# Kernel optimization log

Measured on AMD Instinct MI355X. Metric: run time of the kernel, lower is better.

## Reference

```python
import jax, jax.numpy as jnp
import numpy as np

L, B, D, H = 128, 4, 768, 300
NT, NR = 7, 12  # ner tags, relation types
EPS = 1e-5


def _cummax(v):
    # torch: cumsum(softmax(v, -1), -1)
    return jnp.cumsum(jax.nn.softmax(v, axis=-1), axis=-1)


def _layernorm(v, g, b):
    mu = jnp.mean(v, axis=-1, keepdims=True)
    var = jnp.var(v, axis=-1, keepdims=True)
    return (v - mu) * jax.lax.rsqrt(var + EPS) * g + b


def setup_inputs() -> dict:
    key = jax.random.key(0)
    ks = jax.random.split(key, 24)
    s = lambda fan_in: 1.0 / np.sqrt(fan_in)
    u = lambda k, shape, sc: jax.random.uniform(k, shape, jnp.float32, -sc, sc)
    inp = {
        "x": jax.random.normal(ks[0], (L, B, D), jnp.float32),
        "mask": jnp.ones((L, B), jnp.float32),
        # PFN_Unit
        "W_ih": u(ks[1], (5 * H, D), s(D)), "b_ih": u(ks[2], (5 * H,), s(D)),
        "W_hh": u(ks[3], (5 * H, H), s(H)), "b_hh": u(ks[4], (5 * H,), s(H)),
        "W_tr": u(ks[5], (H, 3 * H), s(3 * H)), "b_tr": u(ks[6], (H,), s(3 * H)),
        # NERUnit
        "n_W": u(ks[7], (H, 2 * H), s(2 * H)), "n_b": u(ks[8], (H,), s(2 * H)),
        "ner_hW": u(ks[9], (H, 3 * H), s(3 * H)), "ner_hb": u(ks[10], (H,), s(3 * H)),
        "ner_g": jnp.ones((H,), jnp.float32), "ner_beta": jnp.zeros((H,), jnp.float32),
        "ner_tW": u(ks[11], (NT, H), s(H)), "ner_tb": u(ks[12], (NT,), s(H)),
        # ReUnit
        "r_W": u(ks[13], (H, 2 * H), s(2 * H)), "r_b": u(ks[14], (H,), s(2 * H)),
        "re_hW": u(ks[15], (H, 3 * H), s(3 * H)), "re_hb": u(ks[16], (H,), s(3 * H)),
        "re_g": jnp.ones((H,), jnp.float32), "re_beta": jnp.zeros((H,), jnp.float32),
        "re_tW": u(ks[17], (NR, H), s(H)), "re_tb": u(ks[18], (NR,), s(H)),
    }
    return inp


def _encoder(x, W_ih, b_ih, W_hh, b_hh, W_tr, b_tr):
    pre = jnp.einsum('lbd,gd->lbg', x, W_ih) + b_ih  # precompute input transform [L,B,5H]

    def step(carry, gx):
        h, c_in = carry
        gates = gx + h @ W_hh.T + b_hh
        c, eg_cin, rg_cin, eg_c, rg_c = jnp.split(gates, 5, axis=1)
        eg_cin, rg_cin = 1.0 - _cummax(eg_cin), _cummax(rg_cin)
        eg_c, rg_c = 1.0 - _cummax(eg_c), _cummax(rg_c)
        c = jnp.tanh(c)
        ov_c = rg_c * eg_c
        up_c, dn_c = rg_c - ov_c, eg_c - ov_c
        ov_i = rg_cin * eg_cin
        up_i, dn_i = rg_cin - ov_i, eg_cin - ov_i
        share = ov_i * c_in + ov_c * c
        c_re = up_i * c_in + up_c * c + share
        c_ner = dn_i * c_in + dn_c * c + share
        c_out = jnp.concatenate([c_re, c_ner, share], axis=-1) @ W_tr.T + b_tr
        h_out = jnp.tanh(c_out)
        return (h_out, c_out), (jnp.tanh(c_ner), jnp.tanh(c_re), jnp.tanh(share))

    h0 = jnp.zeros((x.shape[1], W_hh.shape[1]), x.dtype)
    _, (h_ner, h_re, h_share) = jax.lax.scan(step, (h0, h0), pre)
    return h_ner, h_re, h_share  # each [L,B,H]


def _pair_unit(h_task, h_share, mask, gW, gb, hW, hb, ln_g, ln_b, tW, tb, diag):
    length = h_task.shape[0]
    # global feature: tanh(Linear(cat(share, task))), max over time
    h_glob = jnp.tanh(jnp.concatenate([h_share, h_task], axis=-1) @ gW.T + gb)  # [L,B,H]
    g = jnp.max(h_glob, axis=0)  # [B,H]
    # pairwise feature [L,L,B,3H] = cat(start, end, global)
    st = jnp.broadcast_to(h_task[:, None], (length, length) + h_task.shape[1:])
    en = jnp.broadcast_to(h_task[None, :], (length, length) + h_task.shape[1:])
    gb4 = jnp.broadcast_to(g, (length, length) + g.shape)
    feat = jnp.concatenate([st, en, gb4], axis=-1)
    out = _layernorm(feat @ hW.T + hb, ln_g, ln_b)
    out = jax.nn.elu(out)  # eval mode: dropout is identity
    out = jax.nn.sigmoid(out @ tW.T + tb)  # [L,L,B,T]
    # mask
    m = mask[:, None, :] * mask[None, :, :]  # [L,L,B]
    if diag:
        m = m * jnp.triu(jnp.ones((length, length), out.dtype))[:, :, None]
    return out * m[..., None]


def reference(x, mask, W_ih, b_ih, W_hh, b_hh, W_tr, b_tr,
              n_W, n_b, ner_hW, ner_hb, ner_g, ner_beta, ner_tW, ner_tb,
              r_W, r_b, re_hW, re_hb, re_g, re_beta, re_tW, re_tb):
    h_ner, h_re, h_share = _encoder(x, W_ih, b_ih, W_hh, b_hh, W_tr, b_tr)
    ner = _pair_unit(h_ner, h_share, mask, n_W, n_b, ner_hW, ner_hb,
                     ner_g, ner_beta, ner_tW, ner_tb, diag=True)
    re = _pair_unit(h_re, h_share, mask, r_W, r_b, re_hW, re_hb,
                    re_g, re_beta, re_tW, re_tb, diag=False)
    return ner, re
```

## Files before the change

kernel.cpp:

```cpp
#include <hip/hip_runtime.h>

#define LLEN 128
#define BB 4
#define DD 768
#define HH 300
#define G5 1500
#define H3 900
#define NTT 7
#define NRR 12
#define NCHB 10
#define RPB 150
#define OPB 30

#define C_WIH  0
#define C_X    1152000
#define C_WHH2 1545216
#define C_WTR2 1995216
#define F_BIH  2265216
#define F_BTR  2266720
#define F_PRE  2267040
#define F_HG0  (F_PRE)
#define F_HG1  (F_PRE+153600)
#define F_A0   (F_PRE+307200)
#define F_E0   (F_PRE+460800)
#define F_GF0  (F_PRE+616832)
#define F_GF1  (F_PRE+618048)
#define F_HNER (F_PRE+768000)
#define F_HRE  (F_HNER+153600)
#define F_HSH  (F_HRE+153600)
#define F_A1   0
#define F_E1   153600
#define F_AUX  (F_HSH+153600)
#define P_CPUB 192000
#define AUXB   2432
#define AUX_FL 9728
#define WS_NEED_BYTES ((size_t)(F_AUX+11776)*4)

typedef unsigned short u16;
typedef unsigned int u32;
typedef float f4 __attribute__((ext_vector_type(4)));
typedef int i4 __attribute__((ext_vector_type(4)));

__device__ __forceinline__ float bf2f(u16 u) {
  union { u32 i; float f; } v; v.i = ((u32)u) << 16; return v.f;
}
__device__ __forceinline__ u16 f2bf(float f) {
  union { float f; u32 i; } v; v.f = f;
  u32 r = v.i + 0x7fffu + ((v.i >> 16) & 1u);
  return (u16)(r >> 16);
}
__device__ __forceinline__ float ldin(const void* p, int i, bool f32) {
  return f32 ? ((const float*)p)[i] : bf2f(((const u16*)p)[i]);
}
__device__ __forceinline__ bool is32(const void* mk) {
  return ((const u16*)mk)[0] == 0;
}
__device__ __forceinline__ float wsum(float x) {
  #pragma unroll
  for (int d = 1; d < 64; d <<= 1) x += __shfl_xor(x, d);
  return x;
}
__device__ __forceinline__ void astore(float* p, float v) {
  union { float f; int i; } u; u.f = v;
  __hip_atomic_store((int*)p, u.i, __ATOMIC_RELAXED, __HIP_MEMORY_SCOPE_AGENT);
}
__device__ __forceinline__ void gbar(int* flag, int tid, int target) {
  __syncthreads();
  if (tid == 0) {
    __builtin_amdgcn_s_waitcnt(0);
    __hip_atomic_fetch_add(flag, 1, __ATOMIC_RELAXED, __HIP_MEMORY_SCOPE_AGENT);
    int it = 0;
    while (__hip_atomic_load(flag, __ATOMIC_RELAXED, __HIP_MEMORY_SCOPE_AGENT) < target) {
      __builtin_amdgcn_s_sleep(1);
      if (++it > 50000) break;
    }
  }
  __syncthreads();
}
__device__ __forceinline__ f4 ld4x(const f4* p, int mode) {
  f4 v;
  if (mode)
    asm volatile("global_load_dwordx4 %0, %1, off sc0\n\ts_waitcnt vmcnt(0)"
                 : "=v"(v) : "v"(p) : "memory");
  else
    asm volatile("global_load_dwordx4 %0, %1, off sc0 sc1\n\ts_waitcnt vmcnt(0)"
                 : "=v"(v) : "v"(p) : "memory");
  return v;
}
__device__ __forceinline__ float ld1x(const float* p, int mode) {
  float v;
  if (mode)
    asm volatile("global_load_dword %0, %1, off sc0\n\ts_waitcnt vmcnt(0)"
                 : "=v"(v) : "v"(p) : "memory");
  else
    asm volatile("global_load_dword %0, %1, off sc0 sc1\n\ts_waitcnt vmcnt(0)"
                 : "=v"(v) : "v"(p) : "memory");
  return v;
}
__device__ __forceinline__ int ldix(const int* p, int mode) {
  int v;
  if (mode)
    asm volatile("global_load_dword %0, %1, off sc0\n\ts_waitcnt vmcnt(0)"
                 : "=v"(v) : "v"(p) : "memory");
  else
    asm volatile("global_load_dword %0, %1, off sc0 sc1\n\ts_waitcnt vmcnt(0)"
                 : "=v"(v) : "v"(p) : "memory");
  return v;
}
__device__ __forceinline__ void exst(float* p, float v, int mode) {
  if (mode) *p = v; else astore(p, v);
}
__device__ __forceinline__ void ld9(const float* base,
                                    f4& a0, f4& a1, f4& a2, f4& a3, f4& a4,
                                    f4& a5, f4& a6, f4& a7, f4& a8) {
  asm volatile(
    "global_load_dwordx4 %0, %9, off sc0\n\t"
    "global_load_dwordx4 %1, %9, off offset:16 sc0\n\t"
    "global_load_dwordx4 %2, %9, off offset:32 sc0\n\t"
    "global_load_dwordx4 %3, %9, off offset:64 sc0\n\t"
    "global_load_dwordx4 %4, %9, off offset:80 sc0\n\t"
    "global_load_dwordx4 %5, %9, off offset:96 sc0\n\t"
    "global_load_dwordx4 %6, %9, off offset:128 sc0\n\t"
    "global_load_dwordx4 %7, %9, off offset:144 sc0\n\t"
    "global_load_dwordx4 %8, %9, off offset:160 sc0\n\t"
    "s_waitcnt vmcnt(0)"
    : "=&v"(a0), "=&v"(a1), "=&v"(a2), "=&v"(a3), "=&v"(a4),
      "=&v"(a5), "=&v"(a6), "=&v"(a7), "=&v"(a8)
    : "v"(base) : "memory");
}
__device__ __forceinline__ int poll10(const int* slots, int tok, int mode) {
  i4 a, b, c;
  if (mode)
    asm volatile("global_load_dwordx4 %0, %3, off sc0\n\t"
                 "global_load_dwordx4 %1, %4, off sc0\n\t"
                 "global_load_dwordx4 %2, %5, off sc0\n\t"
                 "s_waitcnt vmcnt(0)"
                 : "=&v"(a), "=&v"(b), "=&v"(c)
                 : "v"(slots), "v"(slots + 4), "v"(slots + 8) : "memory");
  else
    asm volatile("global_load_dwordx4 %0, %3, off sc0 sc1\n\t"
                 "global_load_dwordx4 %1, %4, off sc0 sc1\n\t"
                 "global_load_dwordx4 %2, %5, off sc0 sc1\n\t"
                 "s_waitcnt vmcnt(0)"
                 : "=&v"(a), "=&v"(b), "=&v"(c)
                 : "v"(slots), "v"(slots + 4), "v"(slots + 8) : "memory");
  return (a.x >= tok) & (a.y >= tok) & (a.z >= tok) & (a.w >= tok) &
         (b.x >= tok) & (b.y >= tok) & (b.z >= tok) & (b.w >= tok) &
         (c.x >= tok) & (c.y >= tok);
}
__device__ __forceinline__ void sbar(int* slots, int ch, int tok, int tid, int mode) {
  asm volatile("s_waitcnt vmcnt(0)" ::: "memory");
  __syncthreads();
  if (tid == 0) {
    if (mode) slots[ch] = tok;
    else __hip_atomic_store(slots + ch, tok, __ATOMIC_RELAXED, __HIP_MEMORY_SCOPE_AGENT);
  }
  if (tid < 64) {
    int it = 0;
    while (!poll10(slots, tok, mode)) {
      __builtin_amdgcn_s_sleep(1);
      if (++it > 5000) break;
    }
  }
  __syncthreads();
}
__device__ __forceinline__ void sbarA(int* slots, int* abf, int ch, int tok, int tid,
                                      volatile int* s_fail) {
  asm volatile("s_waitcnt vmcnt(0)" ::: "memory");
  __syncthreads();
  if (tid == 0)
    __hip_atomic_store(slots + ch, tok, __ATOMIC_RELAXED, __HIP_MEMORY_SCOPE_AGENT);
  if (tid < 64) {
    int it = 0;
    while (!poll10(slots, tok, 0)) {
      __builtin_amdgcn_s_sleep(1);
      ++it;
      if ((it & 255) == 0 &&
          __hip_atomic_load(abf, __ATOMIC_RELAXED, __HIP_MEMORY_SCOPE_AGENT) != 0) {
        *s_fail = 1; break;
      }
      if (it > 8000) {
        __hip_atomic_store(abf, 1, __ATOMIC_RELAXED, __HIP_MEMORY_SCOPE_AGENT);
        *s_fail = 1; break;
      }
    }
  }
  __syncthreads();
}
__device__ __forceinline__ int claim_bc(int* cl, int nb) {
  unsigned xcd;
  asm volatile("s_getreg_b32 %0, hwreg(HW_REG_XCC_ID)" : "=s"(xcd));
  xcd &= 7u;
  int rank = __hip_atomic_fetch_add(cl + xcd, 1, __ATOMIC_RELAXED, __HIP_MEMORY_SCOPE_AGENT);
  __hip_atomic_fetch_add(cl + 8, 1, __ATOMIC_RELAXED, __HIP_MEMORY_SCOPE_AGENT);
  int it = 0;
  while (__hip_atomic_load(cl + 8, __ATOMIC_RELAXED, __HIP_MEMORY_SCOPE_AGENT) < nb) {
    __builtin_amdgcn_s_sleep(2);
    if (++it > 100000) break;
  }
  int base = 0;
  for (unsigned x = 0; x < xcd; ++x)
    base += __hip_atomic_load(cl + x, __ATOMIC_RELAXED, __HIP_MEMORY_SCOPE_AGENT) / NCHB;
  int cnt = __hip_atomic_load(cl + xcd, __ATOMIC_RELAXED, __HIP_MEMORY_SCOPE_AGENT);
  int slot = base + rank / NCHB;
  return (rank < (cnt / NCHB) * NCHB && slot < BB) ? (slot * 16 + rank % NCHB) : -1;
}

__global__ void k_canon(const void* xo, const void* mk, const void* Wih, const void* bih,
                        const void* Whh, const void* bhh, const void* Wtr, const void* btr,
                        float* ws) {
  bool f32 = is32(mk);
  int piece = blockIdx.y;
  int i0 = blockIdx.x * 256 + threadIdx.x;
  int stride = gridDim.x * 256;
  switch (piece) {
    case 0: if (!f32) for (int i = i0; i < 1152000; i += stride) ws[C_WIH + i] = ldin(Wih, i, f32); break;
    case 1: if (!f32) for (int i = i0; i < 393216; i += stride) ws[C_X + i] = ldin(xo, i, f32); break;
    case 2: for (int i = i0; i < 225000; i += stride) {
      int k2 = i / G5, out = i - k2 * G5;
      float2 v;
      v.x = ldin(Whh, out * HH + 2 * k2, f32);
      v.y = ldin(Whh, out * HH + 2 * k2 + 1, f32);
      ((float2*)(ws + C_WHH2))[i] = v;
    } break;
    case 3: for (int i = i0; i < 135000; i += stride) {
      int k2 = i / HH, out = i - k2 * HH;
      float2 v;
      v.x = ldin(Wtr, out * H3 + 2 * k2, f32);
      v.y = ldin(Wtr, out * H3 + 2 * k2 + 1, f32);
      ((float2*)(ws + C_WTR2))[i] = v;
    } break;
    case 4: for (int i = i0; i < 1824; i += stride) {
      if (i < 1504) ws[F_BIH + i] = (i < G5) ? ldin(bih, i, f32) + ldin(bhh, i, f32) : 0.f;
      else { int j = i - 1504; ws[F_BTR + j] = (j < HH) ? ldin(btr, j, f32) : 0.f; }
    } break;
    case 5: for (int i = i0; i < 11776; i += stride) {
      if (i < AUX_FL) ws[F_AUX + i] = 0.f;
      else {
        int* ip = (int*)(ws + F_AUX + AUX_FL);
        __hip_atomic_store(ip + (i - AUX_FL), 0, __ATOMIC_RELAXED, __HIP_MEMORY_SCOPE_AGENT);
      }
    } break;
  }
}

__global__ void k_pre2(const void* xo, const void* Wo, const void* mk,
                       const float* cX, const float* cW, const float* biasf, float* pre) {
  bool f32 = is32(mk);
  const float* X = f32 ? (const float*)xo : cX;
  const float* W = f32 ? (const float*)Wo : cW;
  __shared__ __align__(16) float xl[8 * DD];
  int tid = threadIdx.x;
  int lb0 = (blockIdx.x >> 1) * 8;
  int half = blockIdx.x & 1;
  for (int e = tid; e < 8 * DD; e += 256) xl[e] = X[(size_t)lb0 * DD + e];
  __syncthreads();
  for (int j = half * 750 + tid; j < half * 750 + 750; j += 256) {
    const float4* w = (const float4*)(W + (size_t)j * DD);
    float acc[8] = {0.f, 0.f, 0.f, 0.f, 0.f, 0.f, 0.f, 0.f};
    #pragma unroll 2
    for (int k = 0; k < DD / 4; ++k) {
      float4 u = w[k];
      #pragma unroll
      for (int r = 0; r < 8; ++r) {
        const float4 p = *(const float4*)(xl + r * DD + k * 4);
        acc[r] += u.x * p.x + u.y * p.y + u.z * p.z + u.w * p.w;
      }
    }
    float bias = biasf[j];
    #pragma unroll
    for (int r = 0; r < 8; ++r) pre[(size_t)(lb0 + r) * G5 + j] = acc[r] + bias;
  }
}

__global__ void __launch_bounds__(512, 2) k_scanA(const float* pre, const float2* W2h, const float2* W2t,
                                                  const float* btrf, float* hner, float* hre, float* hsh,
                                                  float* aux, float* xw) {
  __shared__ __align__(16) float ga_l[1504];
  __shared__ __align__(16) float vv_l[1204];
  __shared__ __align__(16) float tnh_l[304];
  __shared__ __align__(16) float cat_l[904];
  __shared__ __align__(16) float ci_l[304];
  __shared__ __align__(16) float ps[512];
  __shared__ __align__(16) float h_loc[32];
  __shared__ int s_bc;
  __shared__ int s_fail;
  int tid = threadIdx.x;
  int* ibase = (int*)(aux + AUX_FL);
  if (tid == 0) { s_bc = claim_bc(ibase, (int)gridDim.x); s_fail = 0; }
  __syncthreads();
  int bc = s_bc;
  if (bc < 0) return;
  int b = bc >> 4, ch = bc & 15;
  int* slots = ibase + 32 + b * 64;
  int* abf   = slots + 24;
  int* done  = ibase + 1536;

  if (ch < 2) {
    float* pb0 = xw + (size_t)ch * 96000 + b * 24000;
    for (int i = tid; i < 3000; i += 512) {
      int row = i >> 1, col = 10 + (i & 1);
      pb0[row * 16 + col] = 0.f;
    }
  }

  int o0 = 3 * tid;
  float2 wh2[45];
  if (tid < 500) {
    #pragma unroll
    for (int j = 0; j < 3; ++j)
      #pragma unroll
      for (int kk = 0; kk < 15; ++kk)
        wh2[j * 15 + kk] = W2h[(size_t)(ch * 15 + kk) * G5 + (o0 + j)];
  }
  int o2 = tid % OPB, jj = tid / OPB;
  float2 wt[29];
  int k2b = jj * 29;
  int k2e = (k2b + 29 < 450) ? (k2b + 29) : 450;
  int nk2 = k2e - k2b;
  if (tid < 480) {
    const float2* wp = W2t + (size_t)k2b * HH + (ch * OPB + o2);
    #pragma unroll
    for (int q = 0; q < 29; ++q) if (q < nk2) wt[q] = wp[(size_t)q * HH];
  }
  float pv0 = 0.f, pv1 = 0.f, pv2 = 0.f;
  if (tid < 500) {
    const float* pr = pre + (size_t)b * G5 + o0;
    pv0 = pr[0]; pv1 = pr[1]; pv2 = pr[2];
  }
  __syncthreads();

  for (int t = 0; t < LLEN; ++t) {
    int buf = t & 1;
    float* pb = xw + (size_t)buf * 96000 + b * 24000;
    if (t > 0) {
      if (tid < 500) {
        float2 h2[15];
        #pragma unroll
        for (int kk = 0; kk < 15; ++kk) h2[kk] = *(const float2*)(h_loc + 2 * kk);
        #pragma unroll
        for (int j = 0; j < 3; ++j) {
          float acc = 0.f;
          #pragma unroll
          for (int kk = 0; kk < 15; ++kk)
            acc += wh2[j * 15 + kk].x * h2[kk].x + wh2[j * 15 + kk].y * h2[kk].y;
          pb[(size_t)(o0 + j) * 16 + ch] = acc;
        }
      }
      sbarA(slots, abf, ch, t, tid, &s_fail);
      if (s_fail) return;
      if (tid < 500) {
        f4 a0, a1, a2, a3, a4, a5, a6, a7, a8;
        ld9(pb + (size_t)o0 * 16, a0, a1, a2, a3, a4, a5, a6, a7, a8);
        ga_l[o0]     = pv0 + (((a0.x + a0.y) + (a0.z + a0.w)) +
                              ((a1.x + a1.y) + (a1.z + a1.w)) +
                              ((a2.x + a2.y) + (a2.z + a2.w)));
        ga_l[o0 + 1] = pv1 + (((a3.x + a3.y) + (a3.z + a3.w)) +
                              ((a4.x + a4.y) + (a4.z + a4.w)) +
                              ((a5.x + a5.y) + (a5.z + a5.w)));
        ga_l[o0 + 2] = pv2 + (((a6.x + a6.y) + (a6.z + a6.w)) +
                              ((a7.x + a7.y) + (a7.z + a7.w)) +
                              ((a8.x + a8.y) + (a8.z + a8.w)));
      }
      if (tid < 75) {
        const float* cp = xw + P_CPUB + (size_t)(((t - 1) & 1) * 4 + b) * 304;
        f4 v = ld4x((const f4*)cp + tid, 1);
        *(f4*)(ci_l + 4 * tid) = v;
      }
    } else {
      if (tid < 500) { ga_l[o0] = pv0; ga_l[o0 + 1] = pv1; ga_l[o0 + 2] = pv2; }
    }
    __syncthreads();
    if (tid < HH) tnh_l[tid] = tanhf(ga_l[tid]);
    {
      int w = tid >> 6, ln = tid & 63;
      if (w >= 4) {
        int c = w - 3;
        const float* g = ga_l + c * 300;
        int e0 = ln * 5;
        float ex0 = 0.f, ex1 = 0.f, ex2 = 0.f, ex3 = 0.f, ex4 = 0.f;
        if (ln < 60) {
          ex0 = __expf(g[e0]); ex1 = __expf(g[e0 + 1]); ex2 = __expf(g[e0 + 2]);
          ex3 = __expf(g[e0 + 3]); ex4 = __expf(g[e0 + 4]);
        }
        float p = ((ex0 + ex1) + (ex2 + ex3)) + ex4;
        float inc = p;
        #pragma unroll
        for (int d = 1; d < 64; d <<= 1) { float o = __shfl_up(inc, d); if (ln >= d) inc += o; }
        float S = __shfl(inc, 59);
        float invS = 1.f / S;
        float run = inc - p;
        if (ln < 60) {
          float* vv = vv_l + (c - 1) * 300 + e0;
          run += ex0; vv[0] = run * invS;
          run += ex1; vv[1] = run * invS;
          run += ex2; vv[2] = run * invS;
          run += ex3; vv[3] = run * invS;
          run += ex4; vv[4] = run * invS;
        }
      }
    }
    if (t + 1 < LLEN && tid < 500) {
      const float* pr = pre + ((size_t)(t + 1) * BB + b) * G5 + o0;
      pv0 = pr[0]; pv1 = pr[1]; pv2 = pr[2];
    }
    __syncthreads();
    if (tid < HH) {
      float c = tnh_l[tid];
      float v0 = vv_l[tid], v1 = vv_l[300 + tid], v2 = vv_l[600 + tid], v3 = vv_l[900 + tid];
      float eg_cin = 1.f - v0, rg_cin = v1, eg_c = 1.f - v2, rg_c = v3;
      float ci = (t > 0) ? ci_l[tid] : 0.f;
      float ov_c = rg_c * eg_c;
      float up_c = rg_c - ov_c, dn_c = eg_c - ov_c;
      float ov_i = rg_cin * eg_cin;
      float up_i = rg_cin - ov_i, dn_i = eg_cin - ov_i;
      float share = ov_i * ci + ov_c * c;
      float c_re  = up_i * ci + up_c * c + share;
      float c_ner = dn_i * ci + dn_c * c + share;
      cat_l[tid] = c_re; cat_l[HH + tid] = c_ner; cat_l[2 * HH + tid] = share;
      int sb = ch * OPB;
      if (tid >= sb && tid < sb + OPB) {
        size_t ob = ((size_t)t * BB + b) * HH + tid;
        hner[ob] = tanhf(c_ner); hre[ob] = tanhf(c_re); hsh[ob] = tanhf(share);
      }
    }
    __syncthreads();
    if (tid < 480) {
      float acc = 0.f;
      #pragma unroll
      for (int q = 0; q < 29; ++q)
        if (q < nk2) acc += wt[q].x * cat_l[2 * (k2b + q)] + wt[q].y * cat_l[2 * (k2b + q) + 1];
      ps[tid] = acc;
    }
    __syncthreads();
    if (tid < OPB) {
      float co = btrf[ch * OPB + tid];
      #pragma unroll
      for (int q = 0; q < 16; ++q) co += ps[q * OPB + tid];
      h_loc[tid] = tanhf(co);
      float* cp = xw + P_CPUB + (size_t)(buf * 4 + b) * 304;
      cp[ch * OPB + tid] = co;
    }
    __syncthreads();
  }
  if (tid == 0 && s_fail == 0)
    __hip_atomic_fetch_add(done + b, 1, __ATOMIC_RELAXED, __HIP_MEMORY_SCOPE_AGENT);
}

__global__ void __launch_bounds__(512, 2) k_scanB(const float* pre, const float2* W2h, const float2* W2t,
                                                  const float* btrf, float* hner, float* hre, float* hsh,
                                                  float* aux) {
  __shared__ __align__(16) float h_l[304];
  __shared__ __align__(16) float ci_l[304];
  __shared__ __align__(16) float ga_l[1504];
  __shared__ __align__(16) float cat_l[904];
  __shared__ __align__(16) float ps[512];
  __shared__ __align__(16) float sums_l[8];
  __shared__ float exv[160];
  __shared__ int s_bc, s_mode, s_skip;
  int tid = threadIdx.x;
  int* ibase = (int*)(aux + AUX_FL);
  int* cl2 = ibase + 640;
  if (tid == 0) s_bc = claim_bc(cl2, (int)gridDim.x);
  __syncthreads();
  int bc = s_bc;
  if (bc < 0) return;
  int b = bc >> 4, ch = bc & 15;
  int* done = ibase + 1536;
  if (tid == 0)
    s_skip = (__hip_atomic_load(done + b, __ATOMIC_RELAXED, __HIP_MEMORY_SCOPE_AGENT) == NCHB);
  __syncthreads();
  if (s_skip) return;
  int s = ch >> 1;
  int r0 = ch * RPB;
  float* gb   = aux + b * AUXB;
  float* cb   = gb + 1504;
  float* hb   = gb + 1808;
  float* sums = gb + 2112;
  int* slotsA = ibase + 672 + b * 64;
  int* slotsB = slotsA + 16;
  int* atf    = slotsA + 32;

  {
    float* tst = gb + 2240;
    int* seflag = (int*)(gb + 2272);
    if (ch == 0 && tid == 0) tst[0] = 1.0f;
    gbar(atf + 0, tid, NCHB);
    if (tid == 0) { float w1 = ld1x(tst, 1); (void)w1; }
    gbar(atf + 1, tid, NCHB);
    if (ch == 0 && tid == 0) { tst[0] = 2.0f; __builtin_amdgcn_s_waitcnt(0); }
    if (ch == 1 && tid == 0)
      __hip_atomic_fetch_add(seflag, 1, __ATOMIC_RELAXED, __HIP_MEMORY_SCOPE_WORKGROUP);
    gbar(atf + 2, tid, NCHB);
    if (tid == 0) {
      float w2 = ld1x(tst, 1);
      int fv = ldix(seflag, 1);
      if (w2 != 2.0f || fv != 1)
        __hip_atomic_fetch_or(atf + 4, 1, __ATOMIC_RELAXED, __HIP_MEMORY_SCOPE_AGENT);
    }
    gbar(atf + 3, tid, NCHB);
    if (tid == 0)
      s_mode = (__hip_atomic_load(atf + 4, __ATOMIC_RELAXED, __HIP_MEMORY_SCOPE_AGENT) == 0) ? 1 : 0;
    __syncthreads();
  }
  int mode = s_mode;

  int j = tid / RPB, r = tid - j * RPB;
  int o2 = tid % OPB, jj = tid / OPB;
  int kb = j * 100;

  float2 wh[50];
  if (tid < 450) {
    const float2* wp = W2h + (size_t)(j * 50) * G5 + (r0 + r);
    #pragma unroll
    for (int kk = 0; kk < 50; ++kk) wh[kk] = wp[(size_t)kk * G5];
  }
  float2 wt[29];
  int k2b = jj * 29;
  int k2e = (k2b + 29 < 450) ? (k2b + 29) : 450;
  int nk2 = k2e - k2b;
  if (tid < 480) {
    const float2* wp = W2t + (size_t)k2b * HH + (ch * OPB + o2);
    #pragma unroll
    for (int q = 0; q < 29; ++q) if (q < nk2) wt[q] = wp[(size_t)q * HH];
  }
  float pv = 0.f;
  if (tid < RPB) pv = pre[(size_t)b * G5 + r0 + tid];
  __syncthreads();

  for (int t = 0; t < LLEN; ++t) {
    if (t > 0) {
      if (tid < 75)       { f4 v = ld4x((const f4*)hb + tid, mode); *(f4*)(h_l + 4 * tid) = v; }
      else if (tid < 150) { int q = tid - 75; f4 v = ld4x((const f4*)cb + q, mode); *(f4*)(ci_l + 4 * q) = v; }
      __syncthreads();
    }
    if (tid < 450) {
      float acc = (j == 0) ? pv : 0.f;
      if (t > 0) {
        #pragma unroll
        for (int kk = 0; kk < 50; ++kk)
          acc += wh[kk].x * h_l[kb + 2 * kk] + wh[kk].y * h_l[kb + 2 * kk + 1];
      }
      ps[tid] = acc;
    }
    __syncthreads();
    if (tid < RPB) {
      float g = ps[tid] + ps[RPB + tid] + ps[2 * RPB + tid];
      if (s == 0) exst(gb + r0 + tid, tanhf(g), mode);
      else exv[tid] = __expf(g);
    }
    if (s > 0) {
      __syncthreads();
      if (tid < 30) {
        int base2 = tid * 5;
        float e0 = exv[base2], e1 = exv[base2 + 1], e2 = exv[base2 + 2],
              e3 = exv[base2 + 3], e4 = exv[base2 + 4];
        float p = ((e0 + e1) + (e2 + e3)) + e4;
        float inc = p;
        #pragma unroll
        for (int d = 1; d < 32; d <<= 1) { float o = __shfl_up(inc, d); if (tid >= d) inc += o; }
        float tot = __shfl(inc, 29);
        float run = inc - p;
        run += e0; exst(gb + r0 + base2,     run, mode);
        run += e1; exst(gb + r0 + base2 + 1, run, mode);
        run += e2; exst(gb + r0 + base2 + 2, run, mode);
        run += e3; exst(gb + r0 + base2 + 3, run, mode);
        run += e4; exst(gb + r0 + base2 + 4, run, mode);
        if (tid == 0) exst(sums + (ch - 2), tot, mode);
      }
    }
    sbar(slotsA, ch, t + 1, tid, mode);
    if (tid < 375)      { f4 v = ld4x((const f4*)gb + tid, mode); *(f4*)(ga_l + 4 * tid) = v; }
    else if (tid < 377) { int q = tid - 375; f4 v = ld4x((const f4*)sums + q, mode); *(f4*)(sums_l + 4 * q) = v; }
    float pvn = 0.f;
    if (t + 1 < LLEN && tid < RPB) pvn = pre[((size_t)(t + 1) * BB + b) * G5 + r0 + tid];
    __syncthreads();
    if (tid < HH) {
      float c = ga_l[tid];
      float v[4];
      #pragma unroll
      for (int s1 = 0; s1 < 4; ++s1) {
        float raw = ga_l[(s1 + 1) * HH + tid];
        float off = (tid >= RPB) ? sums_l[2 * s1] : 0.f;
        float S = sums_l[2 * s1] + sums_l[2 * s1 + 1];
        v[s1] = (raw + off) / S;
      }
      float eg_cin = 1.f - v[0], rg_cin = v[1], eg_c = 1.f - v[2], rg_c = v[3];
      float ci = (t > 0) ? ci_l[tid] : 0.f;
      float ov_c = rg_c * eg_c;
      float up_c = rg_c - ov_c, dn_c = eg_c - ov_c;
      float ov_i = rg_cin * eg_cin;
      float up_i = rg_cin - ov_i, dn_i = eg_cin - ov_i;
      float share = ov_i * ci + ov_c * c;
      float c_re  = up_i * ci + up_c * c + share;
      float c_ner = dn_i * ci + dn_c * c + share;
      cat_l[tid] = c_re; cat_l[HH + tid] = c_ner; cat_l[2 * HH + tid] = share;
      int sb = ch * OPB;
      if (tid >= sb && tid < sb + OPB) {
        size_t ob = ((size_t)t * BB + b) * HH + tid;
        hner[ob] = tanhf(c_ner); hre[ob] = tanhf(c_re); hsh[ob] = tanhf(share);
      }
    }
    __syncthreads();
    if (tid < 480) {
      float acc = 0.f;
      #pragma unroll
      for (int q = 0; q < 29; ++q)
        if (q < nk2) acc += wt[q].x * cat_l[2 * (k2b + q)] + wt[q].y * cat_l[2 * (k2b + q) + 1];
      ps[tid] = acc;
    }
    __syncthreads();
    if (tid < OPB) {
      float co = btrf[ch * OPB + tid];
      #pragma unroll
      for (int q = 0; q < 16; ++q) co += ps[q * OPB + tid];
      exst(cb + ch * OPB + tid, co, mode);
      exst(hb + ch * OPB + tid, tanhf(co), mode);
    }
    if (t + 1 < LLEN) sbar(slotsB, ch, t + 1, tid, mode);
    pv = pvn;
  }
}

__global__ void k_post(const float* hsh, const float* hner, const float* hre,
                       const void* nW, const void* nb, const void* rW, const void* rb,
                       const void* nhW, const void* nhb, const void* rhW, const void* rhb,
                       const void* mk, float* hg0, float* hg1,
                       float* A0, float* E0, float* A1, float* E1) {
  bool f32 = is32(mk);
  int role = blockIdx.x >> 8;
  int sub  = blockIdx.x & 255;
  int task = sub >> 7;
  int lb0 = (sub & 127) * 4;
  __shared__ __align__(16) float buf[2400];
  int tid = threadIdx.x;
  if (role == 0) {
    const float* tsk = task ? hre : hner;
    const void* gWo = task ? rW : nW;
    const void* gbo = task ? rb : nb;
    float* hg = task ? hg1 : hg0;
    for (int e = tid; e < 2400; e += 320) {
      int rr = e / 600, c = e - rr * 600;
      buf[e] = (c < HH) ? hsh[(size_t)(lb0 + rr) * HH + c] : tsk[(size_t)(lb0 + rr) * HH + (c - HH)];
    }
    __syncthreads();
    if (tid < HH) {
      float bias = ldin(gbo, tid, f32);
      float acc[4] = {bias, bias, bias, bias};
      if (f32) {
        const float4* row = (const float4*)((const float*)gWo + (size_t)tid * 600);
        #pragma unroll 2
        for (int k = 0; k < 150; ++k) {
          float4 u = row[k];
          #pragma unroll
          for (int rr = 0; rr < 4; ++rr) {
            const float4 cv = *(const float4*)(buf + rr * 600 + 4 * k);
            acc[rr] += u.x * cv.x + u.y * cv.y + u.z * cv.z + u.w * cv.w;
          }
        }
      } else {
        for (int k = 0; k < 600; ++k) {
          float w = ldin(gWo, tid * 600 + k, f32);
          #pragma unroll
          for (int rr = 0; rr < 4; ++rr) acc[rr] += w * buf[rr * 600 + k];
        }
      }
      #pragma unroll
      for (int rr = 0; rr < 4; ++rr) hg[(size_t)(lb0 + rr) * HH + tid] = tanhf(acc[rr]);
    }
  } else {
    const float* tsk = task ? hre : hner;
    const void* hWo = task ? rhW : nhW;
    const void* hbo = task ? rhb : nhb;
    float* A = task ? A1 : A0;
    float* E = task ? E1 : E0;
    for (int e = tid; e < 1200; e += 320) {
      int rr = e / 300, c = e - rr * 300;
      buf[e] = tsk[(size_t)(lb0 + rr) * HH + c];
    }
    __syncthreads();
    if (tid < HH) {
      float bias = ldin(hbo, tid, f32);
      float a[4] = {bias, bias, bias, bias};
      float ev[4] = {0.f, 0.f, 0.f, 0.f};
      if (f32) {
        const float4* r1 = (const float4*)((const float*)hWo + (size_t)tid * H3);
        const float4* r2 = (const float4*)((const float*)hWo + (size_t)tid * H3 + HH);
        #pragma unroll 2
        for (int k = 0; k < 75; ++k) {
          float4 u = r1[k], w2 = r2[k];
          #pragma unroll
          for (int rr = 0; rr < 4; ++rr) {
            const float4 tv = *(const float4*)(buf + rr * 300 + 4 * k);
            a[rr]  += u.x * tv.x + u.y * tv.y + u.z * tv.z + u.w * tv.w;
            ev[rr] += w2.x * tv.x + w2.y * tv.y + w2.z * tv.z + w2.w * tv.w;
          }
        }
      } else {
        for (int k = 0; k < HH; ++k) {
          float w1 = ldin(hWo, tid * H3 + k, f32);
          float w2 = ldin(hWo, tid * H3 + HH + k, f32);
          #pragma unroll
          for (int rr = 0; rr < 4; ++rr) {
            a[rr] += w1 * buf[rr * 300 + k];
            ev[rr] += w2 * buf[rr * 300 + k];
          }
        }
      }
      #pragma unroll
      for (int rr = 0; rr < 4; ++rr) {
        A[(size_t)(lb0 + rr) * HH + tid] = a[rr];
        E[(size_t)(lb0 + rr) * HH + tid] = ev[rr];
      }
    }
  }
}

__global__ void k_gmf(const float* hg0, const float* hg1, const void* nhW, const void* rhW,
                      const void* mk, float* Gf0, float* Gf1) {
  bool f32 = is32(mk);
  int task = blockIdx.x >> 2, b = blockIdx.x & 3;
  const float* hg = task ? hg1 : hg0;
  const void* hWo = task ? rhW : nhW;
  float* Gf = task ? Gf1 : Gf0;
  __shared__ __align__(16) float gl[304];
  int tid = threadIdx.x;
  if (tid < HH) {
    float m = -1e30f;
    for (int l = 0; l < LLEN; ++l) m = fmaxf(m, hg[((size_t)l * BB + b) * HH + tid]);
    gl[tid] = m;
  }
  __syncthreads();
  if (tid < HH) {
    float acc = 0.f;
    if (f32) {
      const float4* row = (const float4*)((const float*)hWo + (size_t)tid * H3 + 600);
      #pragma unroll 5
      for (int k = 0; k < 75; ++k) {
        float4 u = row[k];
        const float4 gv = *(const float4*)(gl + 4 * k);
        acc += u.x * gv.x + u.y * gv.y + u.z * gv.z + u.w * gv.w;
      }
    } else {
      for (int k = 0; k < HH; ++k) acc += gl[k] * ldin(hWo, tid * H3 + 600 + k, f32);
    }
    Gf[b * HH + tid] = acc;
  }
}

__global__ void __launch_bounds__(256) k_pair7(const float* A0, const float* E0, const float* Gf0,
                                               const void* lg0, const void* lb0_, const void* tW0, const void* tb0,
                                               const float* A1, const float* E1, const float* Gf1,
                                               const void* lg1, const void* lb1_, const void* tW1, const void* tb1,
                                               const void* mk, void* outv) {
  __shared__ float lg_l[304], lb_l[304], tb_l[16];
  __shared__ float tw_l[3616];
  bool f32 = is32(mk);
  int tau = blockIdx.x >> 11;
  int bid = blockIdx.x & 2047;
  int i = bid >> 4;
  int j0 = (bid & 15) << 3;
  int T = tau ? NRR : NTT;
  int diag = tau ? 0 : 1;
  int Toff = tau ? 458752 : 0;
  int tid = threadIdx.x;
  int b = tid >> 6, ln = tid & 63;
  if (diag && j0 + 7 < i) {
    if (ln < T) {
      #pragma unroll
      for (int dj = 0; dj < 8; ++dj) {
        size_t obase = (size_t)Toff + ((size_t)(i * LLEN + j0 + dj) * BB + b) * T;
        if (f32) ((float*)outv)[obase + ln] = 0.f;
        else ((u16*)outv)[obase + ln] = 0;
      }
    }
    return;
  }
  const float* A  = tau ? A1 : A0;
  const float* E  = tau ? E1 : E0;
  const float* Gf = tau ? Gf1 : Gf0;
  const void* lgo = tau ? lg1 : lg0;
  const void* lbo = tau ? lb1_ : lb0_;
  const void* tWo = tau ? tW1 : tW0;
  const void* tbo = tau ? tb1 : tb0;
  for (int i2 = tid; i2 < HH; i2 += 256) { lg_l[i2] = ldin(lgo, i2, f32); lb_l[i2] = ldin(lbo, i2, f32); }
  for (int i2 = tid; i2 < T * HH; i2 += 256) tw_l[i2] = ldin(tWo, i2, f32);
  if (tid < T) tb_l[tid] = ldin(tbo, tid, f32);
  __syncthreads();
  const float* ar = A  + (size_t)(i * BB + b) * HH;
  const float* gr = Gf + (size_t)b * HH;
  bool ok4 = ln < 44;
  float a0 = ar[ln]       + gr[ln];
  float a1 = ar[64 + ln]  + gr[64 + ln];
  float a2 = ar[128 + ln] + gr[128 + ln];
  float a3 = ar[192 + ln] + gr[192 + ln];
  float a4 = ok4 ? (ar[256 + ln] + gr[256 + ln]) : 0.f;
  float mi = ldin(mk, i * BB + b, f32);
  for (int dj = 0; dj < 8; ++dj) {
    int jx = j0 + dj;
    const float* er = E + (size_t)(jx * BB + b) * HH;
    float u0 = a0 + er[ln];
    float u1 = a1 + er[64 + ln];
    float u2 = a2 + er[128 + ln];
    float u3 = a3 + er[192 + ln];
    float u4 = ok4 ? (a4 + er[256 + ln]) : 0.f;
    float s1 = ((u0 + u1) + (u2 + u3)) + u4;
    float s2 = ((u0 * u0 + u1 * u1) + (u2 * u2 + u3 * u3)) + u4 * u4;
    #pragma unroll
    for (int d = 1; d < 64; d <<= 1) { s1 += __shfl_xor(s1, d); s2 += __shfl_xor(s2, d); }
    float mean = s1 * (1.f / 300.f);
    float var = s2 * (1.f / 300.f) - mean * mean;
    float rstd = rsqrtf(var + 1e-5f);
    {
      float y;
      y = (u0 - mean) * rstd * lg_l[ln]       + lb_l[ln];       u0 = (y > 0.f) ? y : __expf(y) - 1.f;
      y = (u1 - mean) * rstd * lg_l[64 + ln]  + lb_l[64 + ln];  u1 = (y > 0.f) ? y : __expf(y) - 1.f;
      y = (u2 - mean) * rstd * lg_l[128 + ln] + lb_l[128 + ln]; u2 = (y > 0.f) ? y : __expf(y) - 1.f;
      y = (u3 - mean) * rstd * lg_l[192 + ln] + lb_l[192 + ln]; u3 = (y > 0.f) ? y : __expf(y) - 1.f;
      if (ok4) {
        y = (u4 - mean) * rstd * lg_l[256 + ln] + lb_l[256 + ln];
        u4 = (y > 0.f) ? y : __expf(y) - 1.f;
      }
    }
    float m = mi * ldin(mk, jx * BB + b, f32);
    if (diag && jx < i) m = 0.f;
    size_t obase = (size_t)Toff + ((size_t)(i * LLEN + jx) * BB + b) * T;
    float mine = 0.f;
    for (int t = 0; t < T; ++t) {
      const float* twr = tw_l + t * HH;
      float s = u0 * twr[ln] + u1 * twr[64 + ln] + u2 * twr[128 + ln] + u3 * twr[192 + ln];
      if (ok4) s += u4 * twr[256 + ln];
      s = wsum(s);
      s += tb_l[t];
      float o = m / (1.f + __expf(-s));
      mine = (ln == t) ? o : mine;
    }
    if (ln < T) {
      if (f32) ((float*)outv)[obase + ln] = mine;
      else ((u16*)outv)[obase + ln] = f2bf(mine);
    }
  }
}

__global__ void k_sent(const void* mk, const void* xo, void* outv, int hostcode) {
  __shared__ int bad;
  if (threadIdx.x == 0) bad = 0;
  __syncthreads();
  bool f32 = is32(mk);
  for (int i = threadIdx.x; i < 4096; i += 256) {
    float v = ldin(xo, i, f32);
    if (!(v == v) || fabsf(v) > 1e6f) bad = 1;
  }
  __syncthreads();
  if (threadIdx.x == 0) {
    float code = (float)hostcode;
    if (bad) code = fmaxf(code, 88.f);
    if (code > 0.f) {
      if (f32) ((float*)outv)[0] = code;
      else ((u16*)outv)[0] = f2bf(code);
    }
  }
}

extern "C" void kernel_launch(void* const* d_in, const int* in_sizes, int n_in,
                              void* d_out, int out_size, void* d_ws, size_t ws_size,
                              hipStream_t stream) {
  const void* x    = d_in[0];
  const void* mask = d_in[1];
  const void* Wih  = d_in[2];
  const void* bih  = d_in[3];
  const void* Whh  = d_in[4];
  const void* bhh  = d_in[5];
  const void* Wtr  = d_in[6];
  const void* btr  = d_in[7];
  const void* nW   = d_in[8];
  const void* nb   = d_in[9];
  const void* nhW  = d_in[10];
  const void* nhb  = d_in[11];
  const void* ng   = d_in[12];
  const void* nbe  = d_in[13];
  const void* ntW  = d_in[14];
  const void* ntb  = d_in[15];
  const void* rW   = d_in[16];
  const void* rb   = d_in[17];
  const void* rhW  = d_in[18];
  const void* rhb  = d_in[19];
  const void* rg   = d_in[20];
  const void* rbe  = d_in[21];
  const void* rtW  = d_in[22];
  const void* rtb  = d_in[23];
  float* ws = (float*)d_ws;

  static const int exp_sz[24] = {393216, 512, 1152000, 1500, 450000, 1500, 270000, 300,
                                 180000, 300, 270000, 300, 300, 300, 2100, 7,
                                 180000, 300, 270000, 300, 300, 300, 3600, 12};
  int hostcode = 0;
  if (n_in != 24) hostcode = 890;
  else {
    for (int ii = 0; ii < 24; ++ii)
      if (in_sizes[ii] != exp_sz[ii]) { hostcode = 900 + ii; break; }
  }
  if (hostcode == 0 && out_size != 1245184) hostcode = 880;
  if (hostcode == 0 && ws_size < WS_NEED_BYTES) hostcode = 1099;

  dim3 gc(512, 6);
  k_canon<<<gc, 256, 0, stream>>>(x, mask, Wih, bih, Whh, bhh, Wtr, btr, ws);
  k_pre2<<<128, 256, 0, stream>>>(x, Wih, mask, ws + C_X, ws + C_WIH, ws + F_BIH, ws + F_PRE);
  k_scanA<<<128, 512, 0, stream>>>(ws + F_PRE, (const float2*)(ws + C_WHH2), (const float2*)(ws + C_WTR2),
                                   ws + F_BTR, ws + F_HNER, ws + F_HRE, ws + F_HSH, ws + F_AUX, ws);
  k_scanB<<<128, 512, 0, stream>>>(ws + F_PRE, (const float2*)(ws + C_WHH2), (const float2*)(ws + C_WTR2),
                                   ws + F_BTR, ws + F_HNER, ws + F_HRE, ws + F_HSH, ws + F_AUX);
  k_post<<<512, 320, 0, stream>>>(ws + F_HSH, ws + F_HNER, ws + F_HRE,
                                  nW, nb, rW, rb, nhW, nhb, rhW, rhb, mask,
                                  ws + F_HG0, ws + F_HG1, ws + F_A0, ws + F_E0, ws + F_A1, ws + F_E1);
  k_gmf<<<8, 320, 0, stream>>>(ws + F_HG0, ws + F_HG1, nhW, rhW, mask, ws + F_GF0, ws + F_GF1);
  k_pair7<<<4096, 256, 0, stream>>>(ws + F_A0, ws + F_E0, ws + F_GF0, ng, nbe, ntW, ntb,
                                    ws + F_A1, ws + F_E1, ws + F_GF1, rg, rbe, rtW, rtb,
                                    mask, d_out);
  k_sent<<<1, 256, 0, stream>>>(mask, x, d_out, hostcode);
}
```

Before: 1.367 ms.

## Fuse input projection into canon kernel and early-exit scanB when all batches done

Moves the input-projection GEMM into the canonicalization kernel as an extra grid row, so one kernel launch and its dependency gap go away. The bf16 path now reads weights directly with packed unpacking instead of first writing float copies of W_ih and x to the workspace. The bias is computed inline, which removes the dependency on the bias canonicalization within the same launch. scanB now checks up front whether every batch finished in scanA and, if so, exits before claiming slots. The risk is that the GEMM blocks now share the launch with the weight transposes and can contend with them.

```diff
diff --git a/kernel.cpp b/kernel.cpp
--- a/kernel.cpp
+++ b/kernel.cpp
@@ -44,6 +44,12 @@
 __device__ __forceinline__ float bf2f(u16 u) {
   union { u32 i; float f; } v; v.i = ((u32)u) << 16; return v.f;
 }
+__device__ __forceinline__ float bflo(u32 u) {
+  union { u32 i; float f; } v; v.i = u << 16; return v.f;
+}
+__device__ __forceinline__ float bfhi(u32 u) {
+  union { u32 i; float f; } v; v.i = u & 0xffff0000u; return v.f;
+}
 __device__ __forceinline__ u16 f2bf(float f) {
   union { float f; u32 i; } v; v.f = f;
   u32 r = v.i + 0x7fffu + ((v.i >> 16) & 1u);
@@ -209,67 +215,85 @@
 __global__ void k_canon(const void* xo, const void* mk, const void* Wih, const void* bih,
                         const void* Whh, const void* bhh, const void* Wtr, const void* btr,
                         float* ws) {
+  __shared__ __align__(16) float xl[8 * DD];
   bool f32 = is32(mk);
   int piece = blockIdx.y;
   int i0 = blockIdx.x * 256 + threadIdx.x;
   int stride = gridDim.x * 256;
   switch (piece) {
-    case 0: if (!f32) for (int i = i0; i < 1152000; i += stride) ws[C_WIH + i] = ldin(Wih, i, f32); break;
-    case 1: if (!f32) for (int i = i0; i < 393216; i += stride) ws[C_X + i] = ldin(xo, i, f32); break;
-    case 2: for (int i = i0; i < 225000; i += stride) {
+    case 0: for (int i = i0; i < 225000; i += stride) {
       int k2 = i / G5, out = i - k2 * G5;
       float2 v;
       v.x = ldin(Whh, out * HH + 2 * k2, f32);
       v.y = ldin(Whh, out * HH + 2 * k2 + 1, f32);
       ((float2*)(ws + C_WHH2))[i] = v;
     } break;
-    case 3: for (int i = i0; i < 135000; i += stride) {
+    case 1: for (int i = i0; i < 135000; i += stride) {
       int k2 = i / HH, out = i - k2 * HH;
       float2 v;
       v.x = ldin(Wtr, out * H3 + 2 * k2, f32);
       v.y = ldin(Wtr, out * H3 + 2 * k2 + 1, f32);
       ((float2*)(ws + C_WTR2))[i] = v;
     } break;
-    case 4: for (int i = i0; i < 1824; i += stride) {
+    case 2: for (int i = i0; i < 1824; i += stride) {
       if (i < 1504) ws[F_BIH + i] = (i < G5) ? ldin(bih, i, f32) + ldin(bhh, i, f32) : 0.f;
       else { int j = i - 1504; ws[F_BTR + j] = (j < HH) ? ldin(btr, j, f32) : 0.f; }
     } break;
-    case 5: for (int i = i0; i < 11776; i += stride) {
+    case 3: for (int i = i0; i < 11776; i += stride) {
       if (i < AUX_FL) ws[F_AUX + i] = 0.f;
       else {
         int* ip = (int*)(ws + F_AUX + AUX_FL);
         __hip_atomic_store(ip + (i - AUX_FL), 0, __ATOMIC_RELAXED, __HIP_MEMORY_SCOPE_AGENT);
       }
     } break;
-  }
-}
-
-__global__ void k_pre2(const void* xo, const void* Wo, const void* mk,
-                       const float* cX, const float* cW, const float* biasf, float* pre) {
-  bool f32 = is32(mk);
-  const float* X = f32 ? (const float*)xo : cX;
-  const float* W = f32 ? (const float*)Wo : cW;
-  __shared__ __align__(16) float xl[8 * DD];
-  int tid = threadIdx.x;
-  int lb0 = (blockIdx.x >> 1) * 8;
-  int half = blockIdx.x & 1;
-  for (int e = tid; e < 8 * DD; e += 256) xl[e] = X[(size_t)lb0 * DD + e];
-  __syncthreads();
-  for (int j = half * 750 + tid; j < half * 750 + 750; j += 256) {
-    const float4* w = (const float4*)(W + (size_t)j * DD);
-    float acc[8] = {0.f, 0.f, 0.f, 0.f, 0.f, 0.f, 0.f, 0.f};
-    #pragma unroll 2
-    for (int k = 0; k < DD / 4; ++k) {
-      float4 u = w[k];
-      #pragma unroll
-      for (int r = 0; r < 8; ++r) {
-        const float4 p = *(const float4*)(xl + r * DD + k * 4);
-        acc[r] += u.x * p.x + u.y * p.y + u.z * p.z + u.w * p.w;
-      }
-    }
-    float bias = biasf[j];
-    #pragma unroll
-    for (int r = 0; r < 8; ++r) pre[(size_t)(lb0 + r) * G5 + j] = acc[r] + bias;
+    case 4: {
+      if (blockIdx.x >= 128) return;
+      int tid = threadIdx.x;
+      int lb0 = ((int)blockIdx.x >> 1) * 8;
+      int half = blockIdx.x & 1;
+      float* pre = ws + F_PRE;
+      if (f32) {
+        const float* X = (const float*)xo;
+        for (int e = tid; e < 8 * DD; e += 256) xl[e] = X[(size_t)lb0 * DD + e];
+      } else {
+        const u16* X = (const u16*)xo;
+        for (int e = tid; e < 8 * DD; e += 256) xl[e] = bf2f(X[(size_t)lb0 * DD + e]);
+      }
+      __syncthreads();
+      for (int j = half * 750 + tid; j < half * 750 + 750; j += 256) {
+        float acc[8] = {0.f, 0.f, 0.f, 0.f, 0.f, 0.f, 0.f, 0.f};
+        if (f32) {
+          const float4* w = (const float4*)((const float*)Wih + (size_t)j * DD);
+          #pragma unroll 2
+          for (int k = 0; k < DD / 4; ++k) {
+            float4 u = w[k];
+            #pragma unroll
+            for (int r = 0; r < 8; ++r) {
+              const float4 p = *(const float4*)(xl + r * DD + k * 4);
+              acc[r] += u.x * p.x + u.y * p.y + u.z * p.z + u.w * p.w;
+            }
+          }
+        } else {
+          const u16* wr = (const u16*)Wih + (size_t)j * DD;
+          #pragma unroll 2
+          for (int k = 0; k < DD; k += 8) {
+            uint4 wv = *(const uint4*)(wr + k);
+            float w0 = bflo(wv.x), w1 = bfhi(wv.x), w2 = bflo(wv.y), w3 = bfhi(wv.y);
+            float w4 = bflo(wv.z), w5 = bfhi(wv.z), w6 = bflo(wv.w), w7 = bfhi(wv.w);
+            #pragma unroll
+            for (int r = 0; r < 8; ++r) {
+              const float4 p1 = *(const float4*)(xl + r * DD + k);
+              const float4 p2 = *(const float4*)(xl + r * DD + k + 4);
+              acc[r] += w0 * p1.x + w1 * p1.y + w2 * p1.z + w3 * p1.w
+                      + w4 * p2.x + w5 * p2.y + w6 * p2.z + w7 * p2.w;
+            }
+          }
+        }
+        float bias = ldin(bih, j, f32) + ldin(bhh, j, f32);
+        #pragma unroll
+        for (int r = 0; r < 8; ++r) pre[(size_t)(lb0 + r) * G5 + j] = acc[r] + bias;
+      }
+    } break;
   }
 }
 
@@ -460,13 +484,22 @@
   __shared__ int s_bc, s_mode, s_skip;
   int tid = threadIdx.x;
   int* ibase = (int*)(aux + AUX_FL);
+  int* done = ibase + 1536;
+  if (tid == 0) {
+    int ok = 1;
+    #pragma unroll
+    for (int q = 0; q < BB; ++q)
+      ok &= (__hip_atomic_load(done + q, __ATOMIC_RELAXED, __HIP_MEMORY_SCOPE_AGENT) == NCHB);
+    s_skip = ok;
+  }
+  __syncthreads();
+  if (s_skip) return;
   int* cl2 = ibase + 640;
   if (tid == 0) s_bc = claim_bc(cl2, (int)gridDim.x);
   __syncthreads();
   int bc = s_bc;
   if (bc < 0) return;
   int b = bc >> 4, ch = bc & 15;
-  int* done = ibase + 1536;
   if (tid == 0)
     s_skip = (__hip_atomic_load(done + b, __ATOMIC_RELAXED, __HIP_MEMORY_SCOPE_AGENT) == NCHB);
   __syncthreads();
@@ -903,9 +936,8 @@
   if (hostcode == 0 && out_size != 1245184) hostcode = 880;
   if (hostcode == 0 && ws_size < WS_NEED_BYTES) hostcode = 1099;
 
-  dim3 gc(512, 6);
+  dim3 gc(512, 5);
   k_canon<<<gc, 256, 0, stream>>>(x, mask, Wih, bih, Whh, bhh, Wtr, btr, ws);
-  k_pre2<<<128, 256, 0, stream>>>(x, Wih, mask, ws + C_X, ws + C_WIH, ws + F_BIH, ws + F_PRE);
   k_scanA<<<128, 512, 0, stream>>>(ws + F_PRE, (const float2*)(ws + C_WHH2), (const float2*)(ws + C_WTR2),
                                    ws + F_BTR, ws + F_HNER, ws + F_HRE, ws + F_HSH, ws + F_AUX, ws);
   k_scanB<<<128, 512, 0, stream>>>(ws + F_PRE, (const float2*)(ws + C_WHH2), (const float2*)(ws + C_WTR2),
```

Result: faster. 1.328 ms (-2.9%).
